# Performance work log

Measured on AMD Instinct MI355X. Metric: run time of the kernel, lower is better.

Reference implementation:

```python
import jax, jax.numpy as jnp
import numpy as np

# NF4 16-level codebook (bitsandbytes values)
NF4_CODEBOOK = jnp.array([
    -1.0, -0.6961928009986877, -0.5250730514526367, -0.39491748809814453,
    -0.28444138169288635, -0.18477343022823334, -0.09105003625154495, 0.0,
    0.07958029955625534, 0.16093020141124725, 0.24611230194568634,
    0.33791524171829224, 0.44070982933044434, 0.5626170039176941,
    0.7229568362236328, 1.0], dtype=jnp.float32)

GROUP = 64      # quant_group_size for NF4
R = 16          # LoRA rank
ALPHA = 16      # lora_alpha -> scaling = ALPHA / R = 1.0
E, H, I, T, TOPK = 8, 2048, 1024, 512, 2


def nf4_dequant_gkn(packed, scales, K, N):
    """packed: [E, K//2, N] uint8-valued ints (two 4-bit codes per byte along K).
    scales: [E, K//GROUP, N] float32 per-group absmax. Returns [E, K, N] fp32."""
    e = packed.shape[0]
    lo = packed & 15
    hi = (packed >> 4) & 15
    codes = jnp.stack([lo, hi], axis=2).reshape(e, K, N)      # interleave along K
    w = NF4_CODEBOOK[codes]                                    # [E, K, N]
    w = w.reshape(e, K // GROUP, GROUP, N) * scales[:, :, None, :]
    return w.reshape(e, K, N)


def setup_inputs() -> dict:
    key = jax.random.key(0)
    ks = jax.random.split(key, 16)
    lora_std = 1.0 / np.sqrt(H)
    return {
        "x": jax.random.normal(ks[0], (T, H), jnp.float32),
        "topk_idx": jax.random.randint(ks[1], (T, TOPK), 0, E, jnp.int32),
        "topk_w": jax.random.uniform(ks[2], (T, TOPK), jnp.float32),
        "gate_packed": jax.random.randint(ks[3], (E, H // 2, I), 0, 256, jnp.int32),
        "gate_scales": jax.random.uniform(ks[4], (E, H // GROUP, I), jnp.float32) * 0.02,
        "up_packed": jax.random.randint(ks[5], (E, H // 2, I), 0, 256, jnp.int32),
        "up_scales": jax.random.uniform(ks[6], (E, H // GROUP, I), jnp.float32) * 0.02,
        "down_packed": jax.random.randint(ks[7], (E, I // 2, H), 0, 256, jnp.int32),
        "down_scales": jax.random.uniform(ks[8], (E, I // GROUP, H), jnp.float32) * 0.02,
        "gate_A": jax.random.normal(ks[9], (E, H, R), jnp.float32) * lora_std,
        "gate_B": jax.random.normal(ks[10], (E, R, I), jnp.float32) * 0.02,
        "up_A": jax.random.normal(ks[11], (E, H, R), jnp.float32) * lora_std,
        "up_B": jax.random.normal(ks[12], (E, R, I), jnp.float32) * 0.02,
        "down_A": jax.random.normal(ks[13], (E, I, R), jnp.float32) * lora_std,
        "down_B": jax.random.normal(ks[14], (E, R, H), jnp.float32) * 0.02,
    }


def reference(x, topk_idx, topk_w, gate_packed, gate_scales, up_packed, up_scales,
              down_packed, down_scales, gate_A, gate_B, up_A, up_B, down_A, down_B):
    scaling = ALPHA / R
    # Dequantized NF4 base + LoRA delta, GKN layout [E, K, N]
    Wg = nf4_dequant_gkn(gate_packed, gate_scales, H, I) + scaling * jnp.einsum('ekr,ern->ekn', gate_A, gate_B)
    Wu = nf4_dequant_gkn(up_packed, up_scales, H, I) + scaling * jnp.einsum('ekr,ern->ekn', up_A, up_B)
    Wd = nf4_dequant_gkn(down_packed, down_scales, I, H) + scaling * jnp.einsum('ekr,ern->ekn', down_A, down_B)
    # Grouped GEMM (dense-over-experts reference): SwiGLU per expert
    g = jnp.einsum('th,ehi->eti', x, Wg)          # [E, T, I]
    u = jnp.einsum('th,ehi->eti', x, Wu)
    h = jax.nn.silu(g) * u
    o = jnp.einsum('eti,eih->eth', h, Wd)         # [E, T, H]
    # Routing combine: per-token per-expert weight from top-k assignments
    w_te = jnp.sum((topk_idx[:, :, None] == jnp.arange(E)) * topk_w[:, :, None], axis=1)  # [T, E]
    return jnp.einsum('eth,te->th', o, w_te)
```

## Files before the change

### kernel.cpp

```cpp
#include <hip/hip_runtime.h>
#include <math.h>

#define NE 8
#define NH 2048
#define NI 1024
#define NT 512
#define NTOPK 2
#define NR 16
#define NGROUP 64
#define NPAIR (NT*NTOPK)

typedef short bf16x8 __attribute__((ext_vector_type(8)));
typedef float f32x16 __attribute__((ext_vector_type(16)));
typedef unsigned int u32;

#define MFMA32 __builtin_amdgcn_mfma_f32_32x32x16_bf16

__device__ const float NF4_TAB[16] = {
    -1.0f, -0.6961928009986877f, -0.5250730514526367f, -0.39491748809814453f,
    -0.28444138169288635f, -0.18477343022823334f, -0.09105003625154495f, 0.0f,
    0.07958029955625534f, 0.16093020141124725f, 0.24611230194568634f,
    0.33791524171829224f, 0.44070982933044434f, 0.5626170039176941f,
    0.7229568362236328f, 1.0f};

#define OFF_EXPOFF 0
#define OFF_TOK    256
#define OFF_EXP    4352
#define OFF_W      8448
#define OFF_XAG    12544
#define OFF_XAU    45312
#define OFF_HA     78080
#define OFF_XB     131072
#define OFF_GU     2228224
#define OFF_HBUF   6422528

__device__ inline u32 f2bf(float f) {
    return (__float_as_uint(f) + 0x8000u) >> 16;
}
__device__ inline u32 bfpack2(float a, float b) {
    return ((__float_as_uint(a) + 0x8000u) >> 16) |
           ((__float_as_uint(b) + 0x8000u) & 0xFFFF0000u);
}
__device__ inline bf16x8 asbf(uint4 w) {
    union { uint4 u; bf16x8 b; } c; c.u = w; return c.b;
}
__device__ inline bf16x8 bfzero() { return asbf(make_uint4(0,0,0,0)); }
__device__ inline float bf2f(u32 v) { return __uint_as_float(v << 16); }

__device__ __forceinline__ void stage16(const void* g, void* l) {
    __builtin_amdgcn_global_load_lds(
        (const __attribute__((address_space(1))) u32*)g,
        (__attribute__((address_space(3))) u32*)l, 16, 0, 0);
}

#define WAIT_PREV_STAGE() asm volatile("s_waitcnt vmcnt(8)" ::: "memory")
#define WAIT_ALL()        asm volatile("s_waitcnt vmcnt(0)" ::: "memory")

__global__ __launch_bounds__(1024) void k_route(const int* __restrict__ idx,
                                                const float* __restrict__ w,
                                                int* expert_off, int* ptok,
                                                int* pexp, float* pw) {
    __shared__ int cnt[NE], off[NE + 1], cur[NE];
    int tid = threadIdx.x;
    if (tid < NE) cnt[tid] = 0;
    __syncthreads();
    int e = idx[tid];
    float wt = w[tid];
    int t = tid >> 1;
    atomicAdd(&cnt[e], 1);
    __syncthreads();
    if (tid == 0) {
        off[0] = 0;
        for (int i = 0; i < NE; i++) off[i + 1] = off[i] + cnt[i];
    }
    __syncthreads();
    if (tid < NE) cur[tid] = off[tid];
    __syncthreads();
    int pos = atomicAdd(&cur[e], 1);
    ptok[pos] = t; pexp[pos] = e; pw[pos] = wt;
    if (tid <= NE) expert_off[tid] = off[tid];
}

__global__ __launch_bounds__(256) void k_xcvt(const float* __restrict__ x,
                                              unsigned short* __restrict__ xb) {
    int i = (blockIdx.x * 256 + threadIdx.x) * 8;
    float4 v0 = *(const float4*)(x + i);
    float4 v1 = *(const float4*)(x + i + 4);
    uint4 w;
    w.x = bfpack2(v0.x, v0.y); w.y = bfpack2(v0.z, v0.w);
    w.z = bfpack2(v1.x, v1.y); w.w = bfpack2(v1.z, v1.w);
    *(uint4*)(xb + i) = w;
}

__global__ __launch_bounds__(256) void k_xA(const float* __restrict__ x,
                                            const float* __restrict__ gA,
                                            const float* __restrict__ uA,
                                            const int* __restrict__ ptok,
                                            const int* __restrict__ pexp,
                                            unsigned short* __restrict__ xAg,
                                            unsigned short* __restrict__ xAu) {
    int p = blockIdx.x;
    int t = ptok[p], e = pexp[p];
    int tid = threadIdx.x;
    int r = tid & 15, ch = tid >> 4;
    const float* xr = x + (size_t)t * NH;
    const float* gAr = gA + (size_t)e * NH * NR;
    const float* uAr = uA + (size_t)e * NH * NR;
    float sg = 0.f, su = 0.f;
    for (int j = ch * 128; j < ch * 128 + 128; ++j) {
        float xv = xr[j];
        sg += xv * gAr[j * NR + r];
        su += xv * uAr[j * NR + r];
    }
    __shared__ float red[2][16][16];
    red[0][ch][r] = sg; red[1][ch][r] = su;
    __syncthreads();
    for (int st = 8; st >= 1; st >>= 1) {
        if (ch < st) {
            red[0][ch][r] += red[0][ch + st][r];
            red[1][ch][r] += red[1][ch + st][r];
        }
        __syncthreads();
    }
    if (tid < 16) {
        xAg[p * NR + tid] = (unsigned short)f2bf(red[0][0][tid]);
        xAu[p * NR + tid] = (unsigned short)f2bf(red[1][0][tid]);
    }
}

__global__ __launch_bounds__(64) void k_gu(
    const unsigned short* __restrict__ xb,
    const int* __restrict__ gpk, const float* __restrict__ gsc,
    const int* __restrict__ upk, const float* __restrict__ usc,
    const float* __restrict__ gB, const float* __restrict__ uB,
    const unsigned short* __restrict__ xAg, const unsigned short* __restrict__ xAu,
    const int* __restrict__ expert_off, const int* __restrict__ ptok,
    unsigned short* __restrict__ gu)
{
    __shared__ u32 lut[256];
    __shared__ u32 code[3][1024];
    __shared__ unsigned short afrag[3][2048];
    __shared__ float sclb[32][32];

    int lane = threadIdx.x;
    int q = lane >> 5, cw = lane & 31;
    for (int i = lane; i < 256; i += 64)
        lut[i] = bfpack2(NF4_TAB[i & 15], NF4_TAB[(i >> 4) & 15]);

    int e = blockIdx.x;
    int c0 = blockIdx.y * 32;
    int mat = blockIdx.z & 1;
    int rt = blockIdx.z >> 1;
    const u32* pk = (const u32*)(mat ? upk : gpk);
    const float* scp = mat ? usc : gsc;
    const float* Bp = mat ? uB : gB;
    const unsigned short* xA = mat ? xAu : xAg;

    int off = expert_off[e];
    int cnt = expert_off[e + 1] - off;
    int colg = c0 + cw;
    const size_t pkb = (size_t)e * (NH / 2) * NI;

    {
        const float* sg = scp + (size_t)e * (NH / NGROUP) * NI + c0;
        #pragma unroll
        for (int g = 0; g < 4; ++g)
            stage16(sg + (size_t)(g * 8 + (lane >> 3)) * NI + ((lane & 7) << 2),
                    &sclb[g * 8][0]);
    }

    const int NS = NH / 64;
    for (int s0 = rt * 32; s0 < cnt; s0 += 128) {
        int rr = s0 + cw; if (rr > cnt - 1) rr = cnt - 1;
        u32 ro = (u32)ptok[off + rr] * (u32)NH;

        auto stage = [&](int b, int k0) {
            int kp0 = k0 >> 1;
            #pragma unroll
            for (int g = 0; g < 4; ++g)
                stage16(pk + pkb + (size_t)(kp0 + (g << 3) + (lane >> 3)) * NI
                            + c0 + ((lane & 7) << 2),
                        &code[b][g << 8]);
            #pragma unroll
            for (int ks = 0; ks < 4; ++ks)
                stage16(xb + ro + k0 + (ks << 4) + (q << 3),
                        &afrag[b][ks << 9]);
        };

        f32x16 acc;
        #pragma unroll
        for (int i = 0; i < 16; ++i) acc[i] = 0.f;

        stage(0, 0);
        stage(1, 64);
        for (int s = 0; s < NS; ++s) {
            if (s + 1 < NS) WAIT_PREV_STAGE(); else WAIT_ALL();
            if (s + 2 < NS) stage((s + 2) % 3, (s + 2) * 64);
            int b = s % 3;
            float scl = sclb[s][cw];
            f32x16 t;
            #pragma unroll
            for (int i = 0; i < 16; ++i) t[i] = 0.f;
            #pragma unroll
            for (int ks = 0; ks < 4; ++ks) {
                bf16x8 a = *(const bf16x8*)&afrag[b][(ks << 9) + (lane << 3)];
                uint4 w4; u32* wp = &w4.x;
                #pragma unroll
                for (int i = 0; i < 4; ++i)
                    wp[i] = lut[code[b][(((ks << 3) + (q << 2) + i) << 5) + cw] & 255];
                t = MFMA32(a, asbf(w4), t, 0, 0, 0);
            }
            #pragma unroll
            for (int i = 0; i < 16; ++i) acc[i] += scl * t[i];
        }

        {
            bf16x8 la = bfzero();
            if (s0 + cw < cnt)
                la = *(const bf16x8*)(xA + (size_t)(off + s0 + cw) * NR + (q << 3));
            const float* Bq = Bp + ((size_t)e * NR + (q << 3)) * NI + colg;
            uint4 w4; u32* wp = &w4.x;
            #pragma unroll
            for (int i = 0; i < 4; ++i)
                wp[i] = bfpack2(Bq[(2 * i) * NI], Bq[(2 * i + 1) * NI]);
            acc = MFMA32(la, asbf(w4), acc, 0, 0, 0);
        }
        unsigned short* outb = gu + (size_t)mat * NPAIR * NI;
        #pragma unroll
        for (int reg = 0; reg < 16; ++reg) {
            int rloc = (reg & 3) + 8 * (reg >> 2) + (q << 2);
            if (s0 + rloc < cnt)
                outb[(size_t)(off + s0 + rloc) * NI + colg] =
                    (unsigned short)f2bf(acc[reg]);
        }
    }
}

__global__ __launch_bounds__(256) void k_swiglu(const unsigned short* __restrict__ gu,
                                                unsigned short* __restrict__ hbuf) {
    int i = (blockIdx.x * 256 + threadIdx.x) * 8;
    uint4 gv = *(const uint4*)(gu + i);
    uint4 uv = *(const uint4*)(gu + (size_t)NPAIR * NI + i);
    const u32* gp = &gv.x; const u32* up = &uv.x;
    uint4 hv; u32* hp = &hv.x;
    #pragma unroll
    for (int j = 0; j < 4; ++j) {
        float g0 = bf2f(gp[j] & 0xFFFFu), g1 = bf2f(gp[j] >> 16);
        float u0 = bf2f(up[j] & 0xFFFFu), u1 = bf2f(up[j] >> 16);
        float h0 = g0 * u0 / (1.f + __expf(-g0));
        float h1 = g1 * u1 / (1.f + __expf(-g1));
        hp[j] = bfpack2(h0, h1);
    }
    *(uint4*)(hbuf + i) = hv;
}

__global__ __launch_bounds__(256) void k_hA(const unsigned short* __restrict__ hbuf,
                                            const float* __restrict__ dA,
                                            const int* __restrict__ pexp,
                                            unsigned short* __restrict__ hA) {
    int p = blockIdx.x;
    int e = pexp[p];
    int tid = threadIdx.x;
    int r = tid & 15, ch = tid >> 4;
    const unsigned short* hr = hbuf + (size_t)p * NI;
    const float* dAr = dA + (size_t)e * NI * NR;
    float sv = 0.f;
    for (int j = ch * 64; j < ch * 64 + 64; ++j) {
        float hv = bf2f(hr[j]);
        sv += hv * dAr[j * NR + r];
    }
    __shared__ float red[16][16];
    red[ch][r] = sv;
    __syncthreads();
    for (int st = 8; st >= 1; st >>= 1) {
        if (ch < st) red[ch][r] += red[ch + st][r];
        __syncthreads();
    }
    if (tid < 16) hA[p * NR + tid] = (unsigned short)f2bf(red[0][tid]);
}

__global__ __launch_bounds__(64) void k_dn(
    const unsigned short* __restrict__ hbuf,
    const int* __restrict__ dpk, const float* __restrict__ dsc,
    const float* __restrict__ dB,
    const unsigned short* __restrict__ hA,
    const int* __restrict__ expert_off, const int* __restrict__ ptok,
    const float* __restrict__ pw,
    float* __restrict__ out)
{
    __shared__ u32 lut[256];
    __shared__ u32 code[3][1024];
    __shared__ unsigned short afrag[3][2048];
    __shared__ float sclb[16][32];

    int lane = threadIdx.x;
    int q = lane >> 5, cw = lane & 31;
    for (int i = lane; i < 256; i += 64)
        lut[i] = bfpack2(NF4_TAB[i & 15], NF4_TAB[(i >> 4) & 15]);

    int e = blockIdx.x;
    int c0 = blockIdx.y * 32;
    int rt = blockIdx.z;
    const u32* pk = (const u32*)dpk;

    int off = expert_off[e];
    int cnt = expert_off[e + 1] - off;
    int colg = c0 + cw;
    const size_t pkb = (size_t)e * (NI / 2) * NH;

    {
        const float* sg = dsc + (size_t)e * (NI / NGROUP) * NH + c0;
        #pragma unroll
        for (int g = 0; g < 2; ++g)
            stage16(sg + (size_t)(g * 8 + (lane >> 3)) * NH + ((lane & 7) << 2),
                    &sclb[g * 8][0]);
    }

    const int NS = NI / 64;
    for (int s0 = rt * 32; s0 < cnt; s0 += 128) {
        int rr = s0 + cw; if (rr > cnt - 1) rr = cnt - 1;
        u32 ro = (u32)(off + rr) * (u32)NI;

        auto stage = [&](int b, int k0) {
            int kp0 = k0 >> 1;
            #pragma unroll
            for (int g = 0; g < 4; ++g)
                stage16(pk + pkb + (size_t)(kp0 + (g << 3) + (lane >> 3)) * NH
                            + c0 + ((lane & 7) << 2),
                        &code[b][g << 8]);
            #pragma unroll
            for (int ks = 0; ks < 4; ++ks)
                stage16(hbuf + ro + k0 + (ks << 4) + (q << 3),
                        &afrag[b][ks << 9]);
        };

        f32x16 acc;
        #pragma unroll
        for (int i = 0; i < 16; ++i) acc[i] = 0.f;

        stage(0, 0);
        stage(1, 64);
        for (int s = 0; s < NS; ++s) {
            if (s + 1 < NS) WAIT_PREV_STAGE(); else WAIT_ALL();
            if (s + 2 < NS) stage((s + 2) % 3, (s + 2) * 64);
            int b = s % 3;
            float scl = sclb[s][cw];
            f32x16 t;
            #pragma unroll
            for (int i = 0; i < 16; ++i) t[i] = 0.f;
            #pragma unroll
            for (int ks = 0; ks < 4; ++ks) {
                bf16x8 a = *(const bf16x8*)&afrag[b][(ks << 9) + (lane << 3)];
                uint4 w4; u32* wp = &w4.x;
                #pragma unroll
                for (int i = 0; i < 4; ++i)
                    wp[i] = lut[code[b][(((ks << 3) + (q << 2) + i) << 5) + cw] & 255];
                t = MFMA32(a, asbf(w4), t, 0, 0, 0);
            }
            #pragma unroll
            for (int i = 0; i < 16; ++i) acc[i] += scl * t[i];
        }

        {
            bf16x8 la = bfzero();
            if (s0 + cw < cnt)
                la = *(const bf16x8*)(hA + (size_t)(off + s0 + cw) * NR + (q << 3));
            const float* Bq = dB + ((size_t)e * NR + (q << 3)) * NH + colg;
            uint4 w4; u32* wp = &w4.x;
            #pragma unroll
            for (int i = 0; i < 4; ++i)
                wp[i] = bfpack2(Bq[(2 * i) * NH], Bq[(2 * i + 1) * NH]);
            acc = MFMA32(la, asbf(w4), acc, 0, 0, 0);
        }
        #pragma unroll
        for (int reg = 0; reg < 16; ++reg) {
            int rloc = (reg & 3) + 8 * (reg >> 2) + (q << 2);
            if (s0 + rloc < cnt) {
                int p = off + s0 + rloc;
                atomicAdd(&out[(size_t)ptok[p] * NH + colg], acc[reg] * pw[p]);
            }
        }
    }
}

extern "C" void kernel_launch(void* const* d_in, const int* in_sizes, int n_in,
                              void* d_out, int out_size, void* d_ws,
                              size_t ws_size, hipStream_t stream) {
    const float* x = (const float*)d_in[0];
    const int* topk_idx = (const int*)d_in[1];
    const float* topk_w = (const float*)d_in[2];
    const int* gate_packed = (const int*)d_in[3];
    const float* gate_scales = (const float*)d_in[4];
    const int* up_packed = (const int*)d_in[5];
    const float* up_scales = (const float*)d_in[6];
    const int* down_packed = (const int*)d_in[7];
    const float* down_scales = (const float*)d_in[8];
    const float* gate_A = (const float*)d_in[9];
    const float* gate_B = (const float*)d_in[10];
    const float* up_A = (const float*)d_in[11];
    const float* up_B = (const float*)d_in[12];
    const float* down_A = (const float*)d_in[13];
    const float* down_B = (const float*)d_in[14];
    float* out = (float*)d_out;

    char* ws = (char*)d_ws;
    int* expert_off = (int*)(ws + OFF_EXPOFF);
    int* ptok = (int*)(ws + OFF_TOK);
    int* pexp = (int*)(ws + OFF_EXP);
    float* pw = (float*)(ws + OFF_W);
    unsigned short* xAg = (unsigned short*)(ws + OFF_XAG);
    unsigned short* xAu = (unsigned short*)(ws + OFF_XAU);
    unsigned short* hA = (unsigned short*)(ws + OFF_HA);
    unsigned short* xb = (unsigned short*)(ws + OFF_XB);
    unsigned short* gu = (unsigned short*)(ws + OFF_GU);
    unsigned short* hbuf = (unsigned short*)(ws + OFF_HBUF);

    hipMemsetAsync(d_out, 0, (size_t)NT * NH * sizeof(float), stream);

    k_route<<<1, 1024, 0, stream>>>(topk_idx, topk_w, expert_off, ptok, pexp, pw);
    k_xcvt<<<(NT * NH) / (256 * 8), 256, 0, stream>>>(x, xb);
    k_xA<<<NPAIR, 256, 0, stream>>>(x, gate_A, up_A, ptok, pexp, xAg, xAu);
    k_gu<<<dim3(NE, NI / 32, 8), 64, 0, stream>>>(
        xb, gate_packed, gate_scales, up_packed, up_scales, gate_B, up_B,
        xAg, xAu, expert_off, ptok, gu);
    k_swiglu<<<(NPAIR * NI) / (256 * 8), 256, 0, stream>>>(gu, hbuf);
    k_hA<<<NPAIR, 256, 0, stream>>>(hbuf, down_A, pexp, hA);
    k_dn<<<dim3(NE, NH / 32, 4), 64, 0, stream>>>(
        hbuf, down_packed, down_scales, down_B, hA, expert_off, ptok, pw, out);
}
```

Measured before the change: 293.5 us.

## Gather activations per pair, swizzle LDS A-tiles, batch LoRA-A projections per expert

A new prep kernel gathers and converts routed token rows into a pair-ordered bf16 buffer, replacing the full-x conversion. The gate/up and down GEMMs then stage each A-tile row as one contiguous 128-byte chunk into LDS using an XOR swizzle, instead of scattered 16-byte reads per lane. This is meant to improve global coalescing and avoid LDS bank conflicts. The LoRA-A projection kernels now handle 16 pairs per block per expert, with each thread looping over the full K dimension and no shared-memory reduction. That launches far fewer blocks and gives each thread long serial loops, which may leave those kernels latency-bound.

```diff
diff --git a/kernel.cpp b/kernel.cpp
--- a/kernel.cpp
+++ b/kernel.cpp
@@ -30,9 +30,9 @@
 #define OFF_XAG    12544
 #define OFF_XAU    45312
 #define OFF_HA     78080
-#define OFF_XB     131072
-#define OFF_GU     2228224
-#define OFF_HBUF   6422528
+#define OFF_XC     131072
+#define OFF_GU     4325376
+#define OFF_HBUF   8519680
 
 __device__ inline u32 f2bf(float f) {
     return (__float_as_uint(f) + 0x8000u) >> 16;
@@ -81,65 +81,63 @@
     if (tid <= NE) expert_off[tid] = off[tid];
 }
 
-__global__ __launch_bounds__(256) void k_xcvt(const float* __restrict__ x,
-                                              unsigned short* __restrict__ xb) {
-    int i = (blockIdx.x * 256 + threadIdx.x) * 8;
-    float4 v0 = *(const float4*)(x + i);
-    float4 v1 = *(const float4*)(x + i + 4);
+__global__ __launch_bounds__(256) void k_prep(const float* __restrict__ x,
+                                              const int* __restrict__ ptok,
+                                              unsigned short* __restrict__ xc) {
+    int p = blockIdx.x;
+    int t = ptok[p];
+    const float* src = x + (size_t)t * NH;
+    unsigned short* dst = xc + (size_t)p * NH;
+    int i = threadIdx.x * 8;
+    float4 v0 = *(const float4*)(src + i);
+    float4 v1 = *(const float4*)(src + i + 4);
     uint4 w;
     w.x = bfpack2(v0.x, v0.y); w.y = bfpack2(v0.z, v0.w);
     w.z = bfpack2(v1.x, v1.y); w.w = bfpack2(v1.z, v1.w);
-    *(uint4*)(xb + i) = w;
-}
-
-__global__ __launch_bounds__(256) void k_xA(const float* __restrict__ x,
+    *(uint4*)(dst + i) = w;
+}
+
+__global__ __launch_bounds__(256) void k_xA(const unsigned short* __restrict__ xc,
                                             const float* __restrict__ gA,
                                             const float* __restrict__ uA,
-                                            const int* __restrict__ ptok,
-                                            const int* __restrict__ pexp,
+                                            const int* __restrict__ expert_off,
                                             unsigned short* __restrict__ xAg,
                                             unsigned short* __restrict__ xAu) {
-    int p = blockIdx.x;
-    int t = ptok[p], e = pexp[p];
+    int e = blockIdx.x;
+    int off = expert_off[e], cnt = expert_off[e + 1] - off;
+    int p0 = blockIdx.y * 16;
+    if (p0 >= cnt) return;
     int tid = threadIdx.x;
-    int r = tid & 15, ch = tid >> 4;
-    const float* xr = x + (size_t)t * NH;
-    const float* gAr = gA + (size_t)e * NH * NR;
-    const float* uAr = uA + (size_t)e * NH * NR;
+    int r = tid & 15, p = tid >> 4;
+    int pcl = p0 + p; if (pcl > cnt - 1) pcl = cnt - 1;
+    const unsigned short* xrow = xc + (size_t)(off + pcl) * NH;
+    const float* gAe = gA + (size_t)e * NH * NR + r;
+    const float* uAe = uA + (size_t)e * NH * NR + r;
     float sg = 0.f, su = 0.f;
-    for (int j = ch * 128; j < ch * 128 + 128; ++j) {
-        float xv = xr[j];
-        sg += xv * gAr[j * NR + r];
-        su += xv * uAr[j * NR + r];
-    }
-    __shared__ float red[2][16][16];
-    red[0][ch][r] = sg; red[1][ch][r] = su;
-    __syncthreads();
-    for (int st = 8; st >= 1; st >>= 1) {
-        if (ch < st) {
-            red[0][ch][r] += red[0][ch + st][r];
-            red[1][ch][r] += red[1][ch + st][r];
-        }
-        __syncthreads();
-    }
-    if (tid < 16) {
-        xAg[p * NR + tid] = (unsigned short)f2bf(red[0][0][tid]);
-        xAu[p * NR + tid] = (unsigned short)f2bf(red[1][0][tid]);
+    for (int k = 0; k < NH; k += 2) {
+        u32 xx = *(const u32*)(xrow + k);
+        float x0 = bf2f(xx & 0xFFFFu), x1 = bf2f(xx >> 16);
+        sg += x0 * gAe[(size_t)k * NR] + x1 * gAe[(size_t)(k + 1) * NR];
+        su += x0 * uAe[(size_t)k * NR] + x1 * uAe[(size_t)(k + 1) * NR];
+    }
+    if (p0 + p < cnt) {
+        xAg[(size_t)(off + p0 + p) * NR + r] = (unsigned short)f2bf(sg);
+        xAu[(size_t)(off + p0 + p) * NR + r] = (unsigned short)f2bf(su);
     }
 }
 
 __global__ __launch_bounds__(64) void k_gu(
-    const unsigned short* __restrict__ xb,
+    const unsigned short* __restrict__ xc,
     const int* __restrict__ gpk, const float* __restrict__ gsc,
     const int* __restrict__ upk, const float* __restrict__ usc,
     const float* __restrict__ gB, const float* __restrict__ uB,
     const unsigned short* __restrict__ xAg, const unsigned short* __restrict__ xAu,
-    const int* __restrict__ expert_off, const int* __restrict__ ptok,
+    const int* __restrict__ expert_off,
     unsigned short* __restrict__ gu)
 {
     __shared__ u32 lut[256];
     __shared__ u32 code[3][1024];
-    __shared__ unsigned short afrag[3][2048];
+    __shared__ unsigned short ax[3][2048];
     __shared__ float sclb[32][32];
 
     int lane = threadIdx.x;
@@ -169,22 +167,28 @@
                     &sclb[g * 8][0]);
     }
 
+    int tr8 = lane >> 3;
+    int cs = (lane & 7) ^ tr8;
+    const size_t wbase = pkb + (size_t)tr8 * NI + c0 + ((lane & 7) << 2);
+
     const int NS = NH / 64;
     for (int s0 = rt * 32; s0 < cnt; s0 += 128) {
-        int rr = s0 + cw; if (rr > cnt - 1) rr = cnt - 1;
-        u32 ro = (u32)ptok[off + rr] * (u32)NH;
+        u32 xbase[4];
+        #pragma unroll
+        for (int g = 0; g < 4; ++g) {
+            int rr = s0 + (g << 3) + tr8; if (rr > cnt - 1) rr = cnt - 1;
+            xbase[g] = (u32)(off + rr) * (u32)NH + (u32)(cs << 3);
+        }
 
         auto stage = [&](int b, int k0) {
             int kp0 = k0 >> 1;
             #pragma unroll
             for (int g = 0; g < 4; ++g)
-                stage16(pk + pkb + (size_t)(kp0 + (g << 3) + (lane >> 3)) * NI
-                            + c0 + ((lane & 7) << 2),
+                stage16(pk + wbase + (size_t)(kp0 + (g << 3)) * NI,
                         &code[b][g << 8]);
             #pragma unroll
-            for (int ks = 0; ks < 4; ++ks)
-                stage16(xb + ro + k0 + (ks << 4) + (q << 3),
-                        &afrag[b][ks << 9]);
+            for (int g = 0; g < 4; ++g)
+                stage16(xc + xbase[g] + k0, &ax[b][g << 9]);
         };
 
         f32x16 acc;
@@ -203,7 +207,8 @@
             for (int i = 0; i < 16; ++i) t[i] = 0.f;
             #pragma unroll
             for (int ks = 0; ks < 4; ++ks) {
-                bf16x8 a = *(const bf16x8*)&afrag[b][(ks << 9) + (lane << 3)];
+                int ch_ = ((ks << 1) | q) ^ (cw & 7);
+                bf16x8 a = *(const bf16x8*)&ax[b][(cw << 6) + (ch_ << 3)];
                 uint4 w4; u32* wp = &w4.x;
                 #pragma unroll
                 for (int i = 0; i < 4; ++i)
@@ -256,27 +261,25 @@
 
 __global__ __launch_bounds__(256) void k_hA(const unsigned short* __restrict__ hbuf,
                                             const float* __restrict__ dA,
-                                            const int* __restrict__ pexp,
+                                            const int* __restrict__ expert_off,
                                             unsigned short* __restrict__ hA) {
-    int p = blockIdx.x;
-    int e = pexp[p];
+    int e = blockIdx.x;
+    int off = expert_off[e], cnt = expert_off[e + 1] - off;
+    int p0 = blockIdx.y * 16;
+    if (p0 >= cnt) return;
     int tid = threadIdx.x;
-    int r = tid & 15, ch = tid >> 4;
-    const unsigned short* hr = hbuf + (size_t)p * NI;
-    const float* dAr = dA + (size_t)e * NI * NR;
-    float sv = 0.f;
-    for (int j = ch * 64; j < ch * 64 + 64; ++j) {
-        float hv = bf2f(hr[j]);
-        sv += hv * dAr[j * NR + r];
-    }
-    __shared__ float red[16][16];
-    red[ch][r] = sv;
-    __syncthreads();
-    for (int st = 8; st >= 1; st >>= 1) {
-        if (ch < st) red[ch][r] += red[ch + st][r];
-        __syncthreads();
-    }
-    if (tid < 16) hA[p * NR + tid] = (unsigned short)f2bf(red[0][tid]);
+    int r = tid & 15, p = tid >> 4;
+    int pcl = p0 + p; if (pcl > cnt - 1) pcl = cnt - 1;
+    const unsigned short* hrow = hbuf + (size_t)(off + pcl) * NI;
+    const float* dAe = dA + (size_t)e * NI * NR + r;
+    float s = 0.f;
+    for (int k = 0; k < NI; k += 2) {
+        u32 xx = *(const u32*)(hrow + k);
+        s += bf2f(xx & 0xFFFFu) * dAe[(size_t)k * NR]
+           + bf2f(xx >> 16) * dAe[(size_t)(k + 1) * NR];
+    }
+    if (p0 + p < cnt)
+        hA[(size_t)(off + p0 + p) * NR + r] = (unsigned short)f2bf(s);
 }
 
 __global__ __launch_bounds__(64) void k_dn(
@@ -290,7 +293,7 @@
 {
     __shared__ u32 lut[256];
     __shared__ u32 code[3][1024];
-    __shared__ unsigned short afrag[3][2048];
+    __shared__ unsigned short ax[3][2048];
     __shared__ float sclb[16][32];
 
     int lane = threadIdx.x;
@@ -316,22 +319,28 @@
                     &sclb[g * 8][0]);
     }
 
+    int tr8 = lane >> 3;
+    int cs = (lane & 7) ^ tr8;
+    const size_t wbase = pkb + (size_t)tr8 * NH + c0 + ((lane & 7) << 2);
+
     const int NS = NI / 64;
     for (int s0 = rt * 32; s0 < cnt; s0 += 128) {
-        int rr = s0 + cw; if (rr > cnt - 1) rr = cnt - 1;
-        u32 ro = (u32)(off + rr) * (u32)NI;
+        u32 xbase[4];
+        #pragma unroll
+        for (int g = 0; g < 4; ++g) {
+            int rr = s0 + (g << 3) + tr8; if (rr > cnt - 1) rr = cnt - 1;
+            xbase[g] = (u32)(off + rr) * (u32)NI + (u32)(cs << 3);
+        }
 
         auto stage = [&](int b, int k0) {
             int kp0 = k0 >> 1;
             #pragma unroll
             for (int g = 0; g < 4; ++g)
-                stage16(pk + pkb + (size_t)(kp0 + (g << 3) + (lane >> 3)) * NH
-                            + c0 + ((lane & 7) << 2),
+                stage16(pk + wbase + (size_t)(kp0 + (g << 3)) * NH,
                         &code[b][g << 8]);
             #pragma unroll
-            for (int ks = 0; ks < 4; ++ks)
-                stage16(hbuf + ro + k0 + (ks << 4) + (q << 3),
-                        &afrag[b][ks << 9]);
+            for (int g = 0; g < 4; ++g)
+                stage16(hbuf + xbase[g] + k0, &ax[b][g << 9]);
         };
 
         f32x16 acc;
@@ -350,7 +359,8 @@
             for (int i = 0; i < 16; ++i) t[i] = 0.f;
             #pragma unroll
             for (int ks = 0; ks < 4; ++ks) {
-                bf16x8 a = *(const bf16x8*)&afrag[b][(ks << 9) + (lane << 3)];
+                int ch_ = ((ks << 1) | q) ^ (cw & 7);
+                bf16x8 a = *(const bf16x8*)&ax[b][(cw << 6) + (ch_ << 3)];
                 uint4 w4; u32* wp = &w4.x;
                 #pragma unroll
                 for (int i = 0; i < 4; ++i)
@@ -411,20 +421,20 @@
     unsigned short* xAg = (unsigned short*)(ws + OFF_XAG);
     unsigned short* xAu = (unsigned short*)(ws + OFF_XAU);
     unsigned short* hA = (unsigned short*)(ws + OFF_HA);
-    unsigned short* xb = (unsigned short*)(ws + OFF_XB);
+    unsigned short* xc = (unsigned short*)(ws + OFF_XC);
     unsigned short* gu = (unsigned short*)(ws + OFF_GU);
     unsigned short* hbuf = (unsigned short*)(ws + OFF_HBUF);
 
     hipMemsetAsync(d_out, 0, (size_t)NT * NH * sizeof(float), stream);
 
     k_route<<<1, 1024, 0, stream>>>(topk_idx, topk_w, expert_off, ptok, pexp, pw);
-    k_xcvt<<<(NT * NH) / (256 * 8), 256, 0, stream>>>(x, xb);
-    k_xA<<<NPAIR, 256, 0, stream>>>(x, gate_A, up_A, ptok, pexp, xAg, xAu);
+    k_prep<<<NPAIR, 256, 0, stream>>>(x, ptok, xc);
+    k_xA<<<dim3(NE, 16), 256, 0, stream>>>(xc, gate_A, up_A, expert_off, xAg, xAu);
     k_gu<<<dim3(NE, NI / 32, 8), 64, 0, stream>>>(
-        xb, gate_packed, gate_scales, up_packed, up_scales, gate_B, up_B,
-        xAg, xAu, expert_off, ptok, gu);
+        xc, gate_packed, gate_scales, up_packed, up_scales, gate_B, up_B,
+        xAg, xAu, expert_off, gu);
     k_swiglu<<<(NPAIR * NI) / (256 * 8), 256, 0, stream>>>(gu, hbuf);
-    k_hA<<<NPAIR, 256, 0, stream>>>(hbuf, down_A, pexp, hA);
+    k_hA<<<dim3(NE, 16), 256, 0, stream>>>(hbuf, down_A, expert_off, hA);
     k_dn<<<dim3(NE, NH / 32, 4), 64, 0, stream>>>(
         hbuf, down_packed, down_scales, down_B, hA, expert_off, ptok, pw, out);
 }
```

After: 377.8 us. 28.7% more time.
